# Optimization experiments

Measured on AMD Instinct MI355X. Metric: run time of the kernel, lower is better.

## Reference

```python
import jax, jax.numpy as jnp
import numpy as np

DN = ('NCHW', 'OIHW', 'NCHW')

def conv2d(x, w, b):
    y = jax.lax.conv_general_dilated(x, w, (1, 1), 'SAME', dimension_numbers=DN)
    return y + b[None, :, None, None]

def deform_conv2d(x, offset, w, b):
    # torchvision DeformConv2d v1: kernel 3x3, stride 1, pad 1, dilation 1, no mask.
    # offset: [B, 18, H, W] ordered (dy0, dx0, dy1, dx1, ...) over row-major kernel taps.
    B, C, H, W = x.shape
    K2 = 9
    ki = (jnp.arange(K2) // 3).astype(x.dtype)  # kernel row index i
    kj = (jnp.arange(K2) % 3).astype(x.dtype)   # kernel col index j
    dy = offset[:, 0::2]  # [B, 9, H, W]
    dx = offset[:, 1::2]
    hh = jnp.arange(H, dtype=x.dtype)
    ww = jnp.arange(W, dtype=x.dtype)
    # sampling positions: p = out_pos - pad + k + offset
    py = hh[None, None, :, None] + ki[None, :, None, None] - 1.0 + dy  # [B,9,H,W]
    px = ww[None, None, None, :] + kj[None, :, None, None] - 1.0 + dx

    xf = x.reshape(B, C, H * W)
    y0 = jnp.floor(py); x0 = jnp.floor(px)
    y1 = y0 + 1.0;      x1 = x0 + 1.0
    wy1 = py - y0; wy0 = 1.0 - wy1
    wx1 = px - x0; wx0 = 1.0 - wx1

    def corner(yc, xc, cw):
        valid = (yc >= 0) & (yc <= H - 1) & (xc >= 0) & (xc <= W - 1)
        yi = jnp.clip(yc, 0, H - 1).astype(jnp.int32)
        xi = jnp.clip(xc, 0, W - 1).astype(jnp.int32)
        idx = yi * W + xi                       # [B,9,H,W]
        v = jax.vmap(lambda img, i: img[:, i])(xf, idx)  # [B,C,9,H,W]
        return v * (cw * valid.astype(x.dtype))[:, None]

    sampled = (corner(y0, x0, wy0 * wx0) + corner(y0, x1, wy0 * wx1)
               + corner(y1, x0, wy1 * wx0) + corner(y1, x1, wy1 * wx1))  # [B,C,9,H,W]
    out = jnp.einsum('bckhw,ock->bohw', sampled, w.reshape(w.shape[0], C, K2))
    return out + b[None, :, None, None]

def setup_inputs() -> dict:
    key = jax.random.key(0)
    ks = jax.random.split(key, 20)
    B, C, H, W = 8, 64, 128, 128
    O = 64
    s = 0.05
    inp = {
        'x': jax.random.normal(ks[0], (B, C, H, W), jnp.float32),
        'bsize': jax.random.uniform(ks[1], (B, 2), jnp.float32),
        # glob: Linear(2,64) -> ReLU -> Linear(64,32)
        'gw1': s * jax.random.normal(ks[2], (64, 2), jnp.float32),
        'gb1': jnp.zeros((64,), jnp.float32),
        'gw2': s * jax.random.normal(ks[3], (32, 64), jnp.float32),
        'gb2': jnp.zeros((32,), jnp.float32),
        # local: Conv2d(C,32,3) -> ReLU -> Conv2d(32,32,3)
        'lw1': s * jax.random.normal(ks[4], (32, C, 3, 3), jnp.float32),
        'lb1': jnp.zeros((32,), jnp.float32),
        'lw2': s * jax.random.normal(ks[5], (32, 32, 3, 3), jnp.float32),
        'lb2': jnp.zeros((32,), jnp.float32),
        # fuse: Conv2d(64,32,3) -> ReLU -> Conv2d(32,18,3)
        'fw1': s * jax.random.normal(ks[6], (32, 64, 3, 3), jnp.float32),
        'fb1': jnp.zeros((32,), jnp.float32),
        'fw2': s * jax.random.normal(ks[7], (18, 32, 3, 3), jnp.float32),
        'fb2': jnp.zeros((18,), jnp.float32),
        # deformable conv weight (copied from the source nn.Conv2d) + its own bias
        'dw': s * jax.random.normal(ks[8], (O, C, 3, 3), jnp.float32),
        'db': jnp.zeros((O,), jnp.float32),
    }
    return inp

def reference(x, bsize, gw1, gb1, gw2, gb2, lw1, lb1, lw2, lb2,
              fw1, fb1, fw2, fb2, dw, db):
    B, C, H, W = x.shape
    # global branch: MLP on box-size -> broadcast over spatial dims
    g = jax.nn.relu(bsize @ gw1.T + gb1) @ gw2.T + gb2          # [B,32]
    g_offset = jnp.broadcast_to(g[:, :, None, None], (B, 32, H, W))
    # local branch
    l_offset = conv2d(jax.nn.relu(conv2d(x, lw1, lb1)), lw2, lb2)  # [B,32,H,W]
    # fuse -> 18 offset channels
    fused = jnp.concatenate((g_offset, l_offset), axis=1)          # [B,64,H,W]
    offset = conv2d(jax.nn.relu(conv2d(fused, fw1, fb1)), fw2, fb2)  # [B,18,H,W]
    fea = deform_conv2d(x, offset, dw, db)
    return jax.nn.relu(fea)
```

## Files before the change

kernel.cpp:

```cpp
#include <hip/hip_runtime.h>

#define BB 8
#define CC 64
#define HH 128
#define WW 128
#define HWSZ (HH*WW)

typedef _Float16 h16;
typedef __attribute__((ext_vector_type(8))) _Float16 h16x8;
typedef __attribute__((ext_vector_type(4))) _Float16 h16x4;
typedef __attribute__((ext_vector_type(2))) _Float16 h16x2;
typedef __attribute__((ext_vector_type(4))) float f32x4;

__device__ __forceinline__ void conv_pack(int j, int NCG, const float* w,
                                          int maxo, h16* dst) {
  int e = j & 7, l4 = (j >> 3) & 3, l15 = (j >> 5) & 15, f = (j >> 9) & 1;
  int cg = (j >> 10) & (NCG - 1), kt = (j >> 10) / NCG;
  int o = f * 16 + l15, c = cg * 32 + l4 * 8 + e;
  int CINw = NCG * 32;
  dst[j] = (o < maxo) ? (h16)w[(o * CINw + c) * 9 + kt] : (h16)0.f;
}

__global__ __launch_bounds__(256) void prep_kernel(
    const float* __restrict__ bsize, const float* __restrict__ gw1,
    const float* __restrict__ gb1, const float* __restrict__ gw2,
    const float* __restrict__ gb2, float* __restrict__ g,
    const float* __restrict__ lw1, const float* __restrict__ lw2,
    const float* __restrict__ fw1, const float* __restrict__ fw2,
    const float* __restrict__ dw, h16* __restrict__ cwq,
    h16* __restrict__ dwq, const float* __restrict__ x,
    h16* __restrict__ xt) {
  __shared__ float hbuf[BB][64];
  const int blk = blockIdx.x;
  const int tid = threadIdx.x;
  if (blk == 0) {
#pragma unroll
    for (int i2 = 0; i2 < 2; ++i2) {
      int idx = i2 * 256 + tid;
      int b = idx >> 6, i = idx & 63;
      float v = fmaf(bsize[b * 2 + 0], gw1[i * 2 + 0],
                     fmaf(bsize[b * 2 + 1], gw1[i * 2 + 1], gb1[i]));
      hbuf[b][i] = fmaxf(v, 0.f);
    }
    __syncthreads();
    int b = tid >> 5, j = tid & 31;
    float acc = gb2[j];
#pragma unroll
    for (int i = 0; i < 64; ++i) acc = fmaf(hbuf[b][i], gw2[j * 64 + i], acc);
    g[b * 32 + j] = acc;
  } else if (blk <= 360) {
    int i = (blk - 1) * 256 + tid;
    if (i < 18432) {
      conv_pack(i, 2, lw1, 32, cwq);
    } else if (i < 27648) {
      conv_pack(i - 18432, 1, lw2, 32, cwq + 18432);
    } else if (i < 46080) {
      conv_pack(i - 27648, 2, fw1, 32, cwq + 27648);
    } else if (i < 55296) {
      conv_pack(i - 46080, 1, fw2, 18, cwq + 46080);
    } else if (i < 55296 + 36864) {
      int j = i - 55296;
      int e = j & 7, l4 = (j >> 3) & 3, l15 = (j >> 5) & 15;
      int og = (j >> 9) & 3, cg = (j >> 11) & 1, kt = j >> 12;
      int o = og * 16 + l15, c = cg * 32 + l4 * 8 + e;
      dwq[j] = (h16)dw[(o * 64 + c) * 9 + kt];
    }
  } else {
    int j = blk - 361;
    int b = (1 + j) & 7;
    int slot = j >> 3;
    int t = b * 16384 + slot * 256 + tid;
    int p = t & 16383;
    const float* xb = x + (size_t)b * 64 * HWSZ + p;
    h16* ob = xt + (size_t)t * 64;
#pragma unroll
    for (int c0 = 0; c0 < 64; c0 += 8) {
      h16x8 v;
#pragma unroll
      for (int i = 0; i < 8; ++i) v[i] = (h16)xb[(size_t)(c0 + i) * HWSZ];
      *(h16x8*)(ob + c0) = v;
    }
  }
}

template <int NCG, bool GFUSE, bool RELU, int OMODE>
__global__ __launch_bounds__(512) void conv_mfma_kernel(
    const h16* __restrict__ in, const h16* __restrict__ cwq,
    const float* __restrict__ bias, const float* __restrict__ g,
    h16* __restrict__ outv) {
  constexpr int CINS = GFUSE ? 32 : NCG * 32;
  constexpr int NS = CINS / 8;
  constexpr int LOG2NS = (NS == 8) ? 3 : 2;
  __shared__ __align__(16) h16 sh[4 * 128 * CINS];
  const int wgid = (blockIdx.x & 7) * 64 + (blockIdx.x >> 3);
  const int b = wgid >> 6;
  const int h0 = (wgid & 63) * 2;
  const int lane = threadIdx.x & 63, wave = threadIdx.x >> 6;
  const int wr = wave >> 2, wv = wave & 3;
  const int h = h0 + wr;
  const int l15 = lane & 15, l4 = lane >> 4;
  const h16* inb = in + (size_t)b * HWSZ * CINS;

  for (int q = threadIdx.x; q < 4 * 128 * NS; q += 512) {
    int s = q & (NS - 1), pr = q >> LOG2NS;
    int r = pr >> 7, px = pr & 127;
    int gy = min(max(h0 - 1 + r, 0), HH - 1);
    h16x8 v = *(const h16x8*)(inb + ((size_t)gy * WW + px) * CINS + s * 8);
    *(h16x8*)(sh + pr * CINS + ((s ^ (px & (NS - 1))) * 8)) = v;
  }

  const h16x8 zfr = {0, 0, 0, 0, 0, 0, 0, 0};
  h16x8 gfr = zfr;
  if (GFUSE) {
#pragma unroll
    for (int i = 0; i < 8; ++i) gfr[i] = (h16)g[b * 32 + l4 * 8 + i];
  }
  __syncthreads();

  f32x4 acc[2][2];
#pragma unroll
  for (int f = 0; f < 2; ++f)
#pragma unroll
    for (int j = 0; j < 2; ++j) acc[f][j] = (f32x4){0.f, 0.f, 0.f, 0.f};

#pragma unroll
  for (int kt = 0; kt < 9; ++kt) {
    const int ki = kt / 3 - 1, kj = kt % 3 - 1;
    const int y = h + ki;
    const bool yok = (unsigned)y < HH;
    const int r = ki + 1 + wr;
    int xs[2];
    bool ok[2];
#pragma unroll
    for (int j = 0; j < 2; ++j) {
      int xx = wv * 32 + j * 16 + l15 + kj;
      ok[j] = yok && ((unsigned)xx < WW);
      xs[j] = min(max(xx, 0), WW - 1);
    }
#pragma unroll
    for (int cg = 0; cg < NCG; ++cg) {
      const h16* aq = cwq + (size_t)((kt * NCG + cg) * 2) * 512 + l15 * 32 + l4 * 8;
      h16x8 afr0 = *(const h16x8*)(aq);
      h16x8 afr1 = *(const h16x8*)(aq + 512);
#pragma unroll
      for (int j = 0; j < 2; ++j) {
        h16x8 bv;
        if (GFUSE && cg == 0) {
          bv = ok[j] ? gfr : zfr;
        } else {
          const int s = (!GFUSE && NCG == 2) ? cg * 4 + l4 : l4;
          h16x8 ld = *(const h16x8*)(sh + (r * 128 + xs[j]) * CINS +
                                     ((s ^ (xs[j] & (NS - 1))) * 8));
          bv = ok[j] ? ld : zfr;
        }
        acc[0][j] = __builtin_amdgcn_mfma_f32_16x16x32_f16(afr0, bv, acc[0][j], 0, 0, 0);
        acc[1][j] = __builtin_amdgcn_mfma_f32_16x16x32_f16(afr1, bv, acc[1][j], 0, 0, 0);
      }
    }
  }
  if (OMODE == 0) {
    h16* ob = outv + (size_t)b * HWSZ * 32;
#pragma unroll
    for (int f = 0; f < 2; ++f)
#pragma unroll
      for (int j = 0; j < 2; ++j) {
        int p = h * WW + wv * 32 + j * 16 + l15;
        int o0 = f * 16 + l4 * 4;
        h16x4 st;
#pragma unroll
        for (int r2 = 0; r2 < 4; ++r2) {
          float v = acc[f][j][r2] + bias[o0 + r2];
          if (RELU) v = fmaxf(v, 0.f);
          st[r2] = (h16)v;
        }
        *(h16x4*)(ob + (size_t)p * 32 + o0) = st;
      }
  } else {
    h16* ob = outv + (size_t)b * HWSZ * 24;
#pragma unroll
    for (int j = 0; j < 2; ++j) {
      int p = h * WW + wv * 32 + j * 16 + l15;
      {
        int o0 = l4 * 4;
        h16x4 st;
#pragma unroll
        for (int r2 = 0; r2 < 4; ++r2) st[r2] = (h16)(acc[0][j][r2] + bias[o0 + r2]);
        *(h16x4*)(ob + (size_t)p * 24 + o0) = st;
      }
      if (l4 == 0) {
        h16x2 st2;
        st2[0] = (h16)(acc[1][j][0] + bias[16]);
        st2[1] = (h16)(acc[1][j][1] + bias[17]);
        *(h16x2*)(ob + (size_t)p * 24 + 16) = st2;
      }
    }
  }
}

__global__ __launch_bounds__(512) void deform_mfma_kernel(
    const h16* __restrict__ xt, const h16* __restrict__ offc,
    const h16* __restrict__ dwq, const float* __restrict__ db,
    float* __restrict__ out) {
  __shared__ __align__(16) h16 sh[6 * 72 * 64];
  const int wgid = (blockIdx.x & 7) * 128 + (blockIdx.x >> 3);
  const int b = wgid >> 7;
  const int rh = wgid & 127;
  const int h0 = (rh >> 1) * 2;
  const int halfx = (rh & 1) * 64;
  const int x_lo = halfx - 4;
  const int lane = threadIdx.x & 63, wave = threadIdx.x >> 6;
  const int wr = wave >> 2, wv = wave & 3;
  const int hrow = h0 + wr;
  const int l15 = lane & 15, l4 = lane >> 4;
  const int wx = halfx + wv * 16;
  const int p0 = hrow * WW + wx;
  const int myw = wx + l15;
  const int mypix = p0 + l15;
  const h16* xb = xt + (size_t)b * HWSZ * 64;

#pragma unroll
  for (int it = 0; it < 7; ++it) {
    int q = it * 512 + threadIdx.x;
    if (q < 3456) {
      int s = q & 7, pr = q >> 3;
      int r = pr / 72, i = pr - r * 72;
      int gy = min(max(h0 - 2 + r, 0), HH - 1);
      int gx = min(max(x_lo + i, 0), WW - 1);
      h16x8 v = *(const h16x8*)(xb + ((size_t)gy * WW + gx) * 64 + s * 8);
      *(h16x8*)(sh + pr * 64 + ((s ^ (i & 7)) * 8)) = v;
    }
  }

  const h16* offp = offc + ((size_t)b * HWSZ + mypix) * 24;
  h16x8 offv0 = *(const h16x8*)(offp);
  h16x8 offv1 = *(const h16x8*)(offp + 8);
  h16x8 offv2 = *(const h16x8*)(offp + 16);
  __syncthreads();

#define OFFE(e) ((e) < 8 ? (float)offv0[(e) & 7] : (e) < 16 ? (float)offv1[(e) & 7] : (float)offv2[(e) & 7])

  f32x4 acc[4];
#pragma unroll
  for (int og = 0; og < 4; ++og) acc[og] = (f32x4){0.f, 0.f, 0.f, 0.f};

  h16x8 pc[2][2][4];
  h16x8 pw[2][8];
  h16   pg[2][4];

#define PREF(kt, par) do {                                                  \
    float py = (float)(hrow + (kt) / 3 - 1) + OFFE(2 * (kt));               \
    float px = (float)(myw + (kt) % 3 - 1) + OFFE(2 * (kt) + 1);            \
    float y0f = floorf(py), x0f = floorf(px);                               \
    float wy1 = py - y0f, wy0 = 1.f - wy1;                                  \
    float wx1 = px - x0f, wx0 = 1.f - wx1;                                  \
    int y0 = (int)y0f, x0i = (int)x0f;                                      \
    int y1 = y0 + 1, x1i = x0i + 1;                                         \
    bool y0ok = (unsigned)y0 < HH, y1ok = (unsigned)y1 < HH;                \
    bool x0ok = (unsigned)x0i < WW, x1ok = (unsigned)x1i < WW;              \
    pg[par][0] = (h16)((y0ok && x0ok) ? wy0 * wx0 : 0.f);                   \
    pg[par][1] = (h16)((y0ok && x1ok) ? wy0 * wx1 : 0.f);                   \
    pg[par][2] = (h16)((y1ok && x0ok) ? wy1 * wx0 : 0.f);                   \
    pg[par][3] = (h16)((y1ok && x1ok) ? wy1 * wx1 : 0.f);                   \
    int y0c = min(max(y0, 0), HH - 1), y1c = min(max(y1, 0), HH - 1);       \
    int x0c = min(max(x0i, 0), WW - 1), x1c = min(max(x1i, 0), WW - 1);     \
    int ty0u = y0c - (h0 - 2), ty1u = y1c - (h0 - 2);                       \
    int tx0u = x0c - x_lo, tx1u = x1c - x_lo;                               \
    bool fast = ((unsigned)ty0u <= 5u) & ((unsigned)ty1u <= 5u) &           \
                ((unsigned)tx0u <= 71u) & ((unsigned)tx1u <= 71u);          \
    int ty0 = min(max(ty0u, 0), 5), ty1 = min(max(ty1u, 0), 5);             \
    int tx0 = min(max(tx0u, 0), 71), tx1 = min(max(tx1u, 0), 71);           \
    int pr00 = (ty0 * 72 + tx0) * 64, pr01 = (ty0 * 72 + tx1) * 64;         \
    int pr10 = (ty1 * 72 + tx0) * 64, pr11 = (ty1 * 72 + tx1) * 64;         \
    int sx0 = (tx0 & 7) * 8, sx1 = (tx1 & 7) * 8;                           \
    _Pragma("unroll")                                                       \
    for (int cg = 0; cg < 2; ++cg) {                                        \
      int sb = (cg * 4 + l4) * 8;                                           \
      pc[par][cg][0] = *(const h16x8*)(sh + pr00 + (sb ^ sx0));             \
      pc[par][cg][1] = *(const h16x8*)(sh + pr01 + (sb ^ sx1));             \
      pc[par][cg][2] = *(const h16x8*)(sh + pr10 + (sb ^ sx0));             \
      pc[par][cg][3] = *(const h16x8*)(sh + pr11 + (sb ^ sx1));             \
    }                                                                       \
    if (!fast) {                                                            \
      int i00 = y0c * WW + x0c, i01 = y0c * WW + x1c;                       \
      int i10 = y1c * WW + x0c, i11 = y1c * WW + x1c;                       \
      _Pragma("unroll")                                                     \
      for (int cg = 0; cg < 2; ++cg) {                                      \
        const h16* cb = xb + cg * 32 + l4 * 8;                              \
        pc[par][cg][0] = *(const h16x8*)(cb + (size_t)i00 * 64);            \
        pc[par][cg][1] = *(const h16x8*)(cb + (size_t)i01 * 64);            \
        pc[par][cg][2] = *(const h16x8*)(cb + (size_t)i10 * 64);            \
        pc[par][cg][3] = *(const h16x8*)(cb + (size_t)i11 * 64);            \
      }                                                                     \
    }                                                                       \
    const h16* wq0 = dwq + ((size_t)((kt) * 2 + 0) * 64 + l15) * 32 + l4 * 8; \
    const h16* wq1 = dwq + ((size_t)((kt) * 2 + 1) * 64 + l15) * 32 + l4 * 8; \
    pw[par][0] = *(const h16x8*)(wq0 + 0 * 512);                            \
    pw[par][1] = *(const h16x8*)(wq0 + 1 * 512);                            \
    pw[par][2] = *(const h16x8*)(wq0 + 2 * 512);                            \
    pw[par][3] = *(const h16x8*)(wq0 + 3 * 512);                            \
    pw[par][4] = *(const h16x8*)(wq1 + 0 * 512);                            \
    pw[par][5] = *(const h16x8*)(wq1 + 1 * 512);                            \
    pw[par][6] = *(const h16x8*)(wq1 + 2 * 512);                            \
    pw[par][7] = *(const h16x8*)(wq1 + 3 * 512);                            \
  } while (0)

#define CONS(par) do {                                                      \
    h16 w00 = pg[par][0], w01 = pg[par][1], w10 = pg[par][2], w11 = pg[par][3]; \
    h16x8 s0 = pc[par][0][0] * w00 + pc[par][0][1] * w01                    \
             + pc[par][0][2] * w10 + pc[par][0][3] * w11;                   \
    h16x8 s1 = pc[par][1][0] * w00 + pc[par][1][1] * w01                    \
             + pc[par][1][2] * w10 + pc[par][1][3] * w11;                   \
    acc[0] = __builtin_amdgcn_mfma_f32_16x16x32_f16(s0, pw[par][0], acc[0], 0, 0, 0); \
    acc[1] = __builtin_amdgcn_mfma_f32_16x16x32_f16(s0, pw[par][1], acc[1], 0, 0, 0); \
    acc[2] = __builtin_amdgcn_mfma_f32_16x16x32_f16(s0, pw[par][2], acc[2], 0, 0, 0); \
    acc[3] = __builtin_amdgcn_mfma_f32_16x16x32_f16(s0, pw[par][3], acc[3], 0, 0, 0); \
    acc[0] = __builtin_amdgcn_mfma_f32_16x16x32_f16(s1, pw[par][4], acc[0], 0, 0, 0); \
    acc[1] = __builtin_amdgcn_mfma_f32_16x16x32_f16(s1, pw[par][5], acc[1], 0, 0, 0); \
    acc[2] = __builtin_amdgcn_mfma_f32_16x16x32_f16(s1, pw[par][6], acc[2], 0, 0, 0); \
    acc[3] = __builtin_amdgcn_mfma_f32_16x16x32_f16(s1, pw[par][7], acc[3], 0, 0, 0); \
  } while (0)

  PREF(0, 0);
  PREF(1, 1);
  CONS(0);
  PREF(2, 0);
  CONS(1);
  PREF(3, 1);
  CONS(0);
  PREF(4, 0);
  CONS(1);
  PREF(5, 1);
  CONS(0);
  PREF(6, 0);
  CONS(1);
  PREF(7, 1);
  CONS(0);
  PREF(8, 0);
  CONS(1);
  CONS(0);
#undef PREF
#undef CONS
#undef OFFE

  __syncthreads();
  float* shf = (float*)sh + wr * (64 * 68);
#pragma unroll
  for (int og = 0; og < 4; ++og) {
    int o = og * 16 + l15;
    float bv = db[o];
    f32x4 st;
#pragma unroll
    for (int r = 0; r < 4; ++r) st[r] = fmaxf(acc[og][r] + bv, 0.f);
    *(f32x4*)(shf + o * 68 + wv * 16 + l4 * 4) = st;
  }
  __syncthreads();
  float* outb = out + (size_t)b * CC * HWSZ + hrow * WW + halfx;
#pragma unroll
  for (int it2 = 0; it2 < 4; ++it2) {
    int o = wv * 16 + it2 * 4 + (lane >> 4);
    int px4 = (lane & 15) * 4;
    f32x4 v = *(const f32x4*)(shf + o * 68 + px4);
    *(f32x4*)(outb + (size_t)o * HWSZ + px4) = v;
  }
}

extern "C" void kernel_launch(void* const* d_in, const int* in_sizes, int n_in,
                              void* d_out, int out_size, void* d_ws, size_t ws_size,
                              hipStream_t stream) {
  const float* x     = (const float*)d_in[0];
  const float* bsize = (const float*)d_in[1];
  const float* gw1   = (const float*)d_in[2];
  const float* gb1   = (const float*)d_in[3];
  const float* gw2   = (const float*)d_in[4];
  const float* gb2   = (const float*)d_in[5];
  const float* lw1   = (const float*)d_in[6];
  const float* lb1   = (const float*)d_in[7];
  const float* lw2   = (const float*)d_in[8];
  const float* lb2   = (const float*)d_in[9];
  const float* fw1   = (const float*)d_in[10];
  const float* fb1   = (const float*)d_in[11];
  const float* fw2   = (const float*)d_in[12];
  const float* fb2   = (const float*)d_in[13];
  const float* dw    = (const float*)d_in[14];
  const float* db    = (const float*)d_in[15];
  float* out = (float*)d_out;

  float* gbuf = (float*)d_ws;
  h16* xt   = (h16*)((char*)d_ws + 2048);
  h16* offc = (h16*)((char*)d_ws + 2048 + (size_t)BB * HWSZ * 64 * 2);
  h16* dwq  = (h16*)((char*)offc + (size_t)BB * HWSZ * 24 * 2);

  h16* loff = (h16*)d_out;
  h16* cwq  = (h16*)d_out + 4194304;
  h16* t12  = (h16*)d_out + 8388608;
  const h16* lw1q = cwq;
  const h16* lw2q = cwq + 18432;
  const h16* fw1q = cwq + 27648;
  const h16* fw2q = cwq + 46080;

  prep_kernel<<<873, 256, 0, stream>>>(bsize, gw1, gb1, gw2, gb2, gbuf,
                                       lw1, lw2, fw1, fw2, dw, cwq, dwq, x, xt);
  conv_mfma_kernel<2, false, true, 0><<<512, 512, 0, stream>>>(
      xt, lw1q, lb1, nullptr, t12);
  conv_mfma_kernel<1, false, false, 0><<<512, 512, 0, stream>>>(
      t12, lw2q, lb2, nullptr, loff);
  conv_mfma_kernel<2, true, true, 0><<<512, 512, 0, stream>>>(
      loff, fw1q, fb1, gbuf, t12);
  conv_mfma_kernel<1, false, false, 1><<<512, 512, 0, stream>>>(
      t12, fw2q, fb2, nullptr, offc);
  deform_mfma_kernel<<<1024, 512, 0, stream>>>(xt, offc, dwq, db, out);
}
```

Measured before the change: 108.0 us.

## Fold spatially-constant global offset channels into precomputed border-aware bias; use direct LDS loads

The global branch's 32 offset channels are constant over space, so their contribution to the fw1 conv is now precomputed as a per-batch bias with nine border cases. Tap sums come from the prep kernel and an extra block of the first conv forms the bias. This halves the input channels of the fw1 conv, which now runs as a one-channel-group kernel. Separately, the global-to-shared tile staging in the conv and deform kernels now uses global_load_lds, and the deform kernel's shared-memory output transpose is dropped in favour of direct stores, which may coalesce less well.

```diff
diff --git a/kernel.cpp b/kernel.cpp
--- a/kernel.cpp
+++ b/kernel.cpp
@@ -11,6 +11,9 @@
 typedef __attribute__((ext_vector_type(4))) _Float16 h16x4;
 typedef __attribute__((ext_vector_type(2))) _Float16 h16x2;
 typedef __attribute__((ext_vector_type(4))) float f32x4;
+
+typedef const __attribute__((address_space(1))) unsigned int* gptr_t;
+typedef __attribute__((address_space(3))) unsigned int* lptr_t;
 
 __device__ __forceinline__ void conv_pack(int j, int NCG, const float* w,
                                           int maxo, h16* dst) {
@@ -28,8 +31,8 @@
     const float* __restrict__ lw1, const float* __restrict__ lw2,
     const float* __restrict__ fw1, const float* __restrict__ fw2,
     const float* __restrict__ dw, h16* __restrict__ cwq,
-    h16* __restrict__ dwq, const float* __restrict__ x,
-    h16* __restrict__ xt) {
+    h16* __restrict__ dwq, float* __restrict__ tsum,
+    const float* __restrict__ x, h16* __restrict__ xt) {
   __shared__ float hbuf[BB][64];
   const int blk = blockIdx.x;
   const int tid = threadIdx.x;
@@ -48,23 +51,43 @@
 #pragma unroll
     for (int i = 0; i < 64; ++i) acc = fmaf(hbuf[b][i], gw2[j * 64 + i], acc);
     g[b * 32 + j] = acc;
-  } else if (blk <= 360) {
+  } else if (blk <= 324) {
     int i = (blk - 1) * 256 + tid;
     if (i < 18432) {
       conv_pack(i, 2, lw1, 32, cwq);
     } else if (i < 27648) {
       conv_pack(i - 18432, 1, lw2, 32, cwq + 18432);
+    } else if (i < 36864) {
+      int j = i - 27648;
+      int e = j & 7, l4 = (j >> 3) & 3, l15 = (j >> 5) & 15, f = (j >> 9) & 1;
+      int kt = j >> 10;
+      int o = f * 16 + l15, c = l4 * 8 + e;
+      cwq[27648 + j] = (h16)fw1[(o * 64 + 32 + c) * 9 + kt];
     } else if (i < 46080) {
-      conv_pack(i - 27648, 2, fw1, 32, cwq + 27648);
-    } else if (i < 55296) {
-      conv_pack(i - 46080, 1, fw2, 18, cwq + 46080);
-    } else if (i < 55296 + 36864) {
-      int j = i - 55296;
+      conv_pack(i - 36864, 1, fw2, 18, cwq + 36864);
+    } else if (i < 82944) {
+      int j = i - 46080;
       int e = j & 7, l4 = (j >> 3) & 3, l15 = (j >> 5) & 15;
       int og = (j >> 9) & 3, cg = (j >> 11) & 1, kt = j >> 12;
       int o = og * 16 + l15, c = cg * 32 + l4 * 8 + e;
       dwq[j] = (h16)dw[(o * 64 + c) * 9 + kt];
     }
+  } else if (blk <= 360) {
+    int idx = (blk - 325) * 256 + tid;
+    int rcc = idx >> 10, rem = idx & 1023;
+    int o = rem >> 5, c = rem & 31;
+    int rc = rcc / 3, cc = rcc - rc * 3;
+    float s = 0.f;
+#pragma unroll
+    for (int ri = 0; ri < 3; ++ri) {
+      if ((rc == 1 && ri == 0) || (rc == 2 && ri == 2)) continue;
+#pragma unroll
+      for (int cj = 0; cj < 3; ++cj) {
+        if ((cc == 1 && cj == 0) || (cc == 2 && cj == 2)) continue;
+        s += fw1[(o * 64 + c) * 9 + ri * 3 + cj];
+      }
+    }
+    tsum[idx] = s;
   } else {
     int j = blk - 361;
     int b = (1 + j) & 7;
@@ -83,14 +106,28 @@
   }
 }
 
-template <int NCG, bool GFUSE, bool RELU, int OMODE>
+template <int NCG, bool GB, bool RELU, int OMODE, bool PROD>
 __global__ __launch_bounds__(512) void conv_mfma_kernel(
     const h16* __restrict__ in, const h16* __restrict__ cwq,
-    const float* __restrict__ bias, const float* __restrict__ g,
-    h16* __restrict__ outv) {
-  constexpr int CINS = GFUSE ? 32 : NCG * 32;
+    const float* __restrict__ bias, h16* __restrict__ outv,
+    const float* __restrict__ gbuf, const float* __restrict__ tsum,
+    float* __restrict__ gbias) {
+  if (PROD && blockIdx.x == 512) {
+    for (int t = threadIdx.x; t < 2304; t += 512) {
+      int b = t / 288, rem = t - b * 288;
+      int rcc = rem >> 5, o = rem & 31;
+      float s = 0.f;
+#pragma unroll
+      for (int c = 0; c < 32; ++c)
+        s += gbuf[b * 32 + c] * tsum[rcc * 1024 + o * 32 + c];
+      gbias[t] = s;
+    }
+    return;
+  }
+  constexpr int CINS = NCG * 32;
   constexpr int NS = CINS / 8;
   constexpr int LOG2NS = (NS == 8) ? 3 : 2;
+  constexpr int NCHUNK = 4 * 128 * NS;
   __shared__ __align__(16) h16 sh[4 * 128 * CINS];
   const int wgid = (blockIdx.x & 7) * 64 + (blockIdx.x >> 3);
   const int b = wgid >> 6;
@@ -101,27 +138,37 @@
   const int l15 = lane & 15, l4 = lane >> 4;
   const h16* inb = in + (size_t)b * HWSZ * CINS;
 
-  for (int q = threadIdx.x; q < 4 * 128 * NS; q += 512) {
-    int s = q & (NS - 1), pr = q >> LOG2NS;
+#pragma unroll
+  for (int it = 0; it < NCHUNK / 512; ++it) {
+    int q = it * 512 + threadIdx.x;
+    int sp = q & (NS - 1), pr = q >> LOG2NS;
     int r = pr >> 7, px = pr & 127;
     int gy = min(max(h0 - 1 + r, 0), HH - 1);
-    h16x8 v = *(const h16x8*)(inb + ((size_t)gy * WW + px) * CINS + s * 8);
-    *(h16x8*)(sh + pr * CINS + ((s ^ (px & (NS - 1))) * 8)) = v;
-  }
-
+    int s = sp ^ (px & (NS - 1));
+    const h16* src = inb + ((size_t)gy * WW + px) * CINS + s * 8;
+    __builtin_amdgcn_global_load_lds(
+        (gptr_t)src, (lptr_t)(sh + (size_t)(it * 512 + wave * 64) * 8), 16, 0, 0);
+  }
+
+  f32x4 acc[2][2];
+  if (GB) {
+    const int rc = (h == 0) ? 1 : ((h == 127) ? 2 : 0);
+#pragma unroll
+    for (int f = 0; f < 2; ++f)
+#pragma unroll
+      for (int j = 0; j < 2; ++j) {
+        int wj = wv * 32 + j * 16 + l15;
+        int cc = (wj == 0) ? 1 : ((wj == 127) ? 2 : 0);
+        acc[f][j] = *(const f32x4*)(gbias + (b * 9 + rc * 3 + cc) * 32 + f * 16 + l4 * 4);
+      }
+  } else {
+#pragma unroll
+    for (int f = 0; f < 2; ++f)
+#pragma unroll
+      for (int j = 0; j < 2; ++j) acc[f][j] = (f32x4){0.f, 0.f, 0.f, 0.f};
+  }
   const h16x8 zfr = {0, 0, 0, 0, 0, 0, 0, 0};
-  h16x8 gfr = zfr;
-  if (GFUSE) {
-#pragma unroll
-    for (int i = 0; i < 8; ++i) gfr[i] = (h16)g[b * 32 + l4 * 8 + i];
-  }
   __syncthreads();
-
-  f32x4 acc[2][2];
-#pragma unroll
-  for (int f = 0; f < 2; ++f)
-#pragma unroll
-    for (int j = 0; j < 2; ++j) acc[f][j] = (f32x4){0.f, 0.f, 0.f, 0.f};
 
 #pragma unroll
   for (int kt = 0; kt < 9; ++kt) {
@@ -144,15 +191,10 @@
       h16x8 afr1 = *(const h16x8*)(aq + 512);
 #pragma unroll
       for (int j = 0; j < 2; ++j) {
-        h16x8 bv;
-        if (GFUSE && cg == 0) {
-          bv = ok[j] ? gfr : zfr;
-        } else {
-          const int s = (!GFUSE && NCG == 2) ? cg * 4 + l4 : l4;
-          h16x8 ld = *(const h16x8*)(sh + (r * 128 + xs[j]) * CINS +
-                                     ((s ^ (xs[j] & (NS - 1))) * 8));
-          bv = ok[j] ? ld : zfr;
-        }
+        const int s = (NCG == 2) ? cg * 4 + l4 : l4;
+        h16x8 ld = *(const h16x8*)(sh + (r * 128 + xs[j]) * CINS +
+                                   ((s ^ (xs[j] & (NS - 1))) * 8));
+        h16x8 bv = ok[j] ? ld : zfr;
         acc[0][j] = __builtin_amdgcn_mfma_f32_16x16x32_f16(afr0, bv, acc[0][j], 0, 0, 0);
         acc[1][j] = __builtin_amdgcn_mfma_f32_16x16x32_f16(afr1, bv, acc[1][j], 0, 0, 0);
       }
@@ -222,12 +264,14 @@
   for (int it = 0; it < 7; ++it) {
     int q = it * 512 + threadIdx.x;
     if (q < 3456) {
-      int s = q & 7, pr = q >> 3;
+      int sp = q & 7, pr = q >> 3;
       int r = pr / 72, i = pr - r * 72;
       int gy = min(max(h0 - 2 + r, 0), HH - 1);
       int gx = min(max(x_lo + i, 0), WW - 1);
-      h16x8 v = *(const h16x8*)(xb + ((size_t)gy * WW + gx) * 64 + s * 8);
-      *(h16x8*)(sh + pr * 64 + ((s ^ (i & 7)) * 8)) = v;
+      int s = sp ^ (i & 7);
+      const h16* src = xb + ((size_t)gy * WW + gx) * 64 + s * 8;
+      __builtin_amdgcn_global_load_lds(
+          (gptr_t)src, (lptr_t)(sh + (size_t)(it * 512 + wave * 64) * 8), 16, 0, 0);
     }
   }
 
@@ -342,8 +386,7 @@
 #undef CONS
 #undef OFFE
 
-  __syncthreads();
-  float* shf = (float*)sh + wr * (64 * 68);
+  float* outb = out + (size_t)b * CC * HWSZ;
 #pragma unroll
   for (int og = 0; og < 4; ++og) {
     int o = og * 16 + l15;
@@ -351,16 +394,7 @@
     f32x4 st;
 #pragma unroll
     for (int r = 0; r < 4; ++r) st[r] = fmaxf(acc[og][r] + bv, 0.f);
-    *(f32x4*)(shf + o * 68 + wv * 16 + l4 * 4) = st;
-  }
-  __syncthreads();
-  float* outb = out + (size_t)b * CC * HWSZ + hrow * WW + halfx;
-#pragma unroll
-  for (int it2 = 0; it2 < 4; ++it2) {
-    int o = wv * 16 + it2 * 4 + (lane >> 4);
-    int px4 = (lane & 15) * 4;
-    f32x4 v = *(const f32x4*)(shf + o * 68 + px4);
-    *(f32x4*)(outb + (size_t)o * HWSZ + px4) = v;
+    *(f32x4*)(outb + (size_t)o * HWSZ + p0 + l4 * 4) = st;
   }
 }
 
@@ -389,24 +423,26 @@
   h16* xt   = (h16*)((char*)d_ws + 2048);
   h16* offc = (h16*)((char*)d_ws + 2048 + (size_t)BB * HWSZ * 64 * 2);
   h16* dwq  = (h16*)((char*)offc + (size_t)BB * HWSZ * 24 * 2);
+  float* tsum  = (float*)((char*)dwq + 36864 * 2);
+  float* gbias = tsum + 9216;
 
   h16* loff = (h16*)d_out;
   h16* cwq  = (h16*)d_out + 4194304;
   h16* t12  = (h16*)d_out + 8388608;
   const h16* lw1q = cwq;
   const h16* lw2q = cwq + 18432;
-  const h16* fw1q = cwq + 27648;
-  const h16* fw2q = cwq + 46080;
+  const h16* fw1h = cwq + 27648;
+  const h16* fw2q = cwq + 36864;
 
   prep_kernel<<<873, 256, 0, stream>>>(bsize, gw1, gb1, gw2, gb2, gbuf,
-                                       lw1, lw2, fw1, fw2, dw, cwq, dwq, x, xt);
-  conv_mfma_kernel<2, false, true, 0><<<512, 512, 0, stream>>>(
-      xt, lw1q, lb1, nullptr, t12);
-  conv_mfma_kernel<1, false, false, 0><<<512, 512, 0, stream>>>(
-      t12, lw2q, lb2, nullptr, loff);
-  conv_mfma_kernel<2, true, true, 0><<<512, 512, 0, stream>>>(
-      loff, fw1q, fb1, gbuf, t12);
-  conv_mfma_kernel<1, false, false, 1><<<512, 512, 0, stream>>>(
-      t12, fw2q, fb2, nullptr, offc);
+                                       lw1, lw2, fw1, fw2, dw, cwq, dwq, tsum, x, xt);
+  conv_mfma_kernel<2, false, true, 0, true><<<513, 512, 0, stream>>>(
+      xt, lw1q, lb1, t12, gbuf, tsum, gbias);
+  conv_mfma_kernel<1, false, false, 0, false><<<512, 512, 0, stream>>>(
+      t12, lw2q, lb2, loff, nullptr, nullptr, nullptr);
+  conv_mfma_kernel<1, true, true, 0, false><<<512, 512, 0, stream>>>(
+      loff, fw1h, fb1, t12, nullptr, nullptr, gbias);
+  conv_mfma_kernel<1, false, false, 1, false><<<512, 512, 0, stream>>>(
+      t12, fw2q, fb2, offc, nullptr, nullptr, nullptr);
   deform_mfma_kernel<<<1024, 512, 0, stream>>>(xt, offc, dwq, db, out);
 }
```

After: 110.2 us. +2.1%, slower.
